# Performance work log

Hardware: AMD Instinct MI355X
Metric: run time of the kernel (lower is better)

## Reference

```python
import jax, jax.numpy as jnp
import numpy as np

C_RED = 8
BN_EPS = 1e-5
NORM_EPS = 1e-6

# pairwise upper-triangular index lists (static, matches torch buffers)
_idx_i, _idx_j = [], []
for _i in range(C_RED):
    for _j in range(_i, C_RED):
        _idx_i.append(_i)
        _idx_j.append(_j)
IDX_I = np.array(_idx_i, dtype=np.int32)
IDX_J = np.array(_idx_j, dtype=np.int32)


def setup_inputs() -> dict:
    key = jax.random.key(0)
    ks = jax.random.split(key, 8)
    B, Cin, H, W = 32, 256, 56, 56
    x = jax.random.normal(ks[0], (B, Cin, H, W), dtype=jnp.float32)
    w_reduce = jax.random.normal(ks[1], (C_RED, Cin, 1, 1), dtype=jnp.float32) * 0.05
    bn_gamma = jax.random.uniform(ks[2], (C_RED,), dtype=jnp.float32, minval=0.5, maxval=1.5)
    bn_beta = jax.random.normal(ks[3], (C_RED,), dtype=jnp.float32) * 0.1
    bn_mean = jax.random.normal(ks[4], (C_RED,), dtype=jnp.float32) * 0.1
    bn_var = jax.random.uniform(ks[5], (C_RED,), dtype=jnp.float32, minval=0.5, maxval=1.5)
    w_dw = jax.random.normal(ks[6], (C_RED, 1, 3, 3), dtype=jnp.float32) * 0.3
    scale = jax.random.uniform(ks[7], (1, C_RED, 1, 1), dtype=jnp.float32, minval=0.5, maxval=1.5)
    return {"x": x, "w_reduce": w_reduce, "bn_gamma": bn_gamma, "bn_beta": bn_beta,
            "bn_mean": bn_mean, "bn_var": bn_var, "w_dw": w_dw, "scale": scale}


def _l2norm_ch(z):
    # F.normalize(p=2, dim=1, eps=1e-6): x / max(||x||_2, eps)
    n = jnp.sqrt(jnp.sum(z * z, axis=1, keepdims=True))
    return z / jnp.maximum(n, NORM_EPS)


def reference(x, w_reduce, bn_gamma, bn_beta, bn_mean, bn_var, w_dw, scale):
    # 1x1 conv (no bias)
    z = jax.lax.conv_general_dilated(x, w_reduce, (1, 1), 'VALID',
                                     dimension_numbers=('NCHW', 'OIHW', 'NCHW'))
    # BatchNorm (inference) + ReLU
    inv = bn_gamma / jnp.sqrt(bn_var + BN_EPS)
    z = z * inv[None, :, None, None] + (bn_beta - bn_mean * inv)[None, :, None, None]
    z = jax.nn.relu(z)
    # depthwise 3x3 twist conv, padding 1, times per-channel scale
    z_twist = jax.lax.conv_general_dilated(z, w_dw, (1, 1), ((1, 1), (1, 1)),
                                           dimension_numbers=('NCHW', 'OIHW', 'NCHW'),
                                           feature_group_count=C_RED) * scale
    z_norm = _l2norm_ch(z)
    z_twist_norm = _l2norm_ch(z_twist)
    # gathered pairwise products over upper-triangular channel pairs
    interactions = jnp.take(z_norm, IDX_I, axis=1) * jnp.take(z_twist_norm, IDX_J, axis=1)
    return jnp.concatenate([z_norm, interactions], axis=1)  # [B, 8+36, H, W]
```

## Files before the change

### kernel.cpp

```cpp
#include <hip/hip_runtime.h>

#define BATCH 32
#define CIN   256
#define CR    8
#define HDIM  56
#define WDIM  56
#define HW    3136
#define COUT  44

#define TILE  256

__device__ __constant__ const int PI36[36] =
    {0,0,0,0,0,0,0,0, 1,1,1,1,1,1,1, 2,2,2,2,2,2, 3,3,3,3,3, 4,4,4,4, 5,5,5, 6,6, 7};
__device__ __constant__ const int PJ36[36] =
    {0,1,2,3,4,5,6,7, 1,2,3,4,5,6,7, 2,3,4,5,6,7, 3,4,5,6,7, 4,5,6,7, 5,6,7, 6,7, 7};

__global__ __launch_bounds__(512, 4) void k1_reduce_bn_relu(
    const float* __restrict__ x, const float* __restrict__ wr,
    const float* __restrict__ gamma, const float* __restrict__ beta,
    const float* __restrict__ mean, const float* __restrict__ var,
    float* __restrict__ z)
{
    const int tid  = threadIdx.x;
    const int lane = tid & 63;
    const int wv   = __builtin_amdgcn_readfirstlane(tid >> 6);
    const int px0  = blockIdx.x * TILE;
    const int gp   = px0 + 4 * lane;
    const int b    = gp / HW;
    const int p    = gp - b * HW;
    const int cin0 = wv * 32;

    const float* __restrict__ xq =
        x + (size_t)b * CIN * HW + (size_t)cin0 * HW + p;

    float acc[4][CR];
#pragma unroll
    for (int q = 0; q < 4; ++q)
#pragma unroll
        for (int c = 0; c < CR; ++c) acc[q][c] = 0.f;

    float4 xa[4], xb[4];
    auto loadx = [&](float4 (&arr)[4], int base) {
#pragma unroll
        for (int j = 0; j < 4; ++j)
            arr[j] = *reinterpret_cast<const float4*>(
                         xq + (size_t)(base + j) * HW);
    };
    auto consume = [&](const float4 (&arr)[4], int base) {
#pragma unroll
        for (int j = 0; j < 4; ++j) {
            const int cin = cin0 + base + j;
            const float px4[4] = {arr[j].x, arr[j].y, arr[j].z, arr[j].w};
#pragma unroll
            for (int c = 0; c < CR; ++c) {
                const float wgt = wr[c * CIN + cin];
#pragma unroll
                for (int q = 0; q < 4; ++q)
                    acc[q][c] = fmaf(px4[q], wgt, acc[q][c]);
            }
        }
    };

    loadx(xa, 0);
    loadx(xb, 4);
#pragma unroll
    for (int k0 = 0; k0 < 32; k0 += 8) {
        consume(xa, k0);
        if (k0 + 8  < 32) loadx(xa, k0 + 8);
        consume(xb, k0 + 4);
        if (k0 + 12 < 32) loadx(xb, k0 + 12);
    }

    __shared__ float pacc[8][CR][TILE];
#pragma unroll
    for (int c = 0; c < CR; ++c)
        *reinterpret_cast<float4*>(&pacc[wv][c][4 * lane]) =
            make_float4(acc[0][c], acc[1][c], acc[2][c], acc[3][c]);
    __syncthreads();

    const int c   = tid >> 6;
    const int pxb = tid & 63;
    const float inv = gamma[c] / sqrtf(var[c] + 1e-5f);
    const float sh  = beta[c] - mean[c] * inv;
#pragma unroll
    for (int k = 0; k < 4; ++k) {
        const int px = pxb + 64 * k;
        float s = 0.f;
#pragma unroll
        for (int w = 0; w < 8; ++w) s += pacc[w][c][px];
        z[(size_t)(px0 + px) * CR + c] = fmaxf(fmaf(s, inv, sh), 0.f);
    }
}

__global__ __launch_bounds__(256) void k2_dw_norm_inter(
    const float* __restrict__ z, const float* __restrict__ wdw,
    const float* __restrict__ scale, float* __restrict__ out)
{
    const int lane = threadIdx.x & 63;
    const int wv   = __builtin_amdgcn_readfirstlane(threadIdx.x >> 6);
    const int t = blockIdx.x * 64 + lane;
    const int b = t / HW;
    const int p = t - b * HW;
    const int h = p / WDIM;
    const int w = p - h * WDIM;

    const float* __restrict__ zimg = z + (size_t)b * HW * CR;

    float4 n0[9], n1[9];
    float  mk[9];
#pragma unroll
    for (int dy = -1; dy <= 1; ++dy) {
#pragma unroll
        for (int dx = -1; dx <= 1; ++dx) {
            const int k  = (dy + 1) * 3 + (dx + 1);
            const int hh = h + dy, ww = w + dx;
            const bool ok = (hh >= 0) & (hh < HDIM) & (ww >= 0) & (ww < WDIM);
            const int hc = min(max(hh, 0), HDIM - 1);
            const int wc = min(max(ww, 0), WDIM - 1);
            mk[k] = ok ? 1.0f : 0.0f;
            const float* zn = zimg + (size_t)(hc * WDIM + wc) * CR;
            n0[k] = reinterpret_cast<const float4*>(zn)[0];
            n1[k] = reinterpret_cast<const float4*>(zn)[1];
        }
    }

    const float zc[CR] = {n0[4].x, n0[4].y, n0[4].z, n0[4].w,
                          n1[4].x, n1[4].y, n1[4].z, n1[4].w};

    float tw[CR];
#pragma unroll
    for (int c = 0; c < CR; ++c) tw[c] = 0.f;
#pragma unroll
    for (int k = 0; k < 9; ++k) {
        const float nv[CR] = {n0[k].x, n0[k].y, n0[k].z, n0[k].w,
                              n1[k].x, n1[k].y, n1[k].z, n1[k].w};
#pragma unroll
        for (int c = 0; c < CR; ++c)
            tw[c] = fmaf(nv[c] * mk[k], wdw[c * 9 + k], tw[c]);
    }

    float s1 = 0.f, s2 = 0.f;
#pragma unroll
    for (int c = 0; c < CR; ++c) {
        tw[c] *= scale[c];
        s1 = fmaf(zc[c], zc[c], s1);
        s2 = fmaf(tw[c], tw[c], s2);
    }
    const float r1 = 1.0f / fmaxf(sqrtf(s1), 1e-6f);
    const float r2 = 1.0f / fmaxf(sqrtf(s2), 1e-6f);

    float a[CR], tb[CR];
#pragma unroll
    for (int c = 0; c < CR; ++c) { a[c] = zc[c] * r1; tb[c] = tw[c] * r2; }

    float* op = out + (size_t)b * COUT * HW + p;
#pragma unroll
    for (int c = 0; c < COUT; ++c) {
        if ((c / 11) == wv) {
            const float val = (c < CR) ? a[c]
                                       : a[PI36[c - CR]] * tb[PJ36[c - CR]];
            op[(size_t)c * HW] = val;
        }
    }
}

extern "C" void kernel_launch(void* const* d_in, const int* in_sizes, int n_in,
                              void* d_out, int out_size, void* d_ws, size_t ws_size,
                              hipStream_t stream) {
    const float* x     = (const float*)d_in[0];
    const float* wr    = (const float*)d_in[1];
    const float* gamma = (const float*)d_in[2];
    const float* beta  = (const float*)d_in[3];
    const float* mean  = (const float*)d_in[4];
    const float* var   = (const float*)d_in[5];
    const float* wdw   = (const float*)d_in[6];
    const float* scale = (const float*)d_in[7];
    float* out = (float*)d_out;
    float* z   = (float*)d_ws;

    const int npix = BATCH * HW;
    k1_reduce_bn_relu<<<npix / TILE, 512, 0, stream>>>(x, wr, gamma, beta, mean, var, z);
    k2_dw_norm_inter<<<npix / 64, 256, 0, stream>>>(z, wdw, scale, out);
}
```

Before: 175.3 us.

## Split reduce conv into per-channel-group partial kernel plus global reduction kernel

Replaces the single reduce+BN kernel with three kernels. A prep kernel transposes the 1x1 weights and precomputes the BN scale and shift. A partial kernel gives each block one batch and one 32-channel group over the whole image, with weights read as float4. A third kernel sums the 8 partials from global memory and applies BN and ReLU. This removes the shared-memory cross-wave reduction and per-block weight gathers, but adds about 25 MB of partial writes and reads to global memory plus two extra launches.

```diff
diff --git a/kernel.cpp b/kernel.cpp
--- a/kernel.cpp
+++ b/kernel.cpp
@@ -8,30 +8,47 @@
 #define HW    3136
 #define COUT  44
 
-#define TILE  256
+#define NCG   8
+#define CPG   32
+#define NPIX  (BATCH*HW)
+#define ZFLT  (NPIX*CR)
+#define F4PP  784
 
 __device__ __constant__ const int PI36[36] =
     {0,0,0,0,0,0,0,0, 1,1,1,1,1,1,1, 2,2,2,2,2,2, 3,3,3,3,3, 4,4,4,4, 5,5,5, 6,6, 7};
 __device__ __constant__ const int PJ36[36] =
     {0,1,2,3,4,5,6,7, 1,2,3,4,5,6,7, 2,3,4,5,6,7, 3,4,5,6,7, 4,5,6,7, 5,6,7, 6,7, 7};
 
-__global__ __launch_bounds__(512, 4) void k1_reduce_bn_relu(
-    const float* __restrict__ x, const float* __restrict__ wr,
-    const float* __restrict__ gamma, const float* __restrict__ beta,
-    const float* __restrict__ mean, const float* __restrict__ var,
-    float* __restrict__ z)
-{
-    const int tid  = threadIdx.x;
-    const int lane = tid & 63;
-    const int wv   = __builtin_amdgcn_readfirstlane(tid >> 6);
-    const int px0  = blockIdx.x * TILE;
-    const int gp   = px0 + 4 * lane;
-    const int b    = gp / HW;
-    const int p    = gp - b * HW;
-    const int cin0 = wv * 32;
-
-    const float* __restrict__ xq =
-        x + (size_t)b * CIN * HW + (size_t)cin0 * HW + p;
+__global__ __launch_bounds__(256) void k0_prep(
+    const float* __restrict__ wr, const float* __restrict__ gamma,
+    const float* __restrict__ beta, const float* __restrict__ mean,
+    const float* __restrict__ var,
+    float* __restrict__ wrT, float* __restrict__ invc, float* __restrict__ shc)
+{
+    const int t = threadIdx.x;
+#pragma unroll
+    for (int c = 0; c < CR; ++c) wrT[t * CR + c] = wr[c * CIN + t];
+    if (t < CR) {
+        const float iv = gamma[t] / sqrtf(var[t] + 1e-5f);
+        invc[t] = iv;
+        shc[t]  = beta[t] - mean[t] * iv;
+    }
+}
+
+__global__ __launch_bounds__(832) void k1a_partial(
+    const float* __restrict__ x, const float* __restrict__ wrT,
+    float* __restrict__ part)
+{
+    const int blk = blockIdx.x;
+    const int b   = blk >> 3;
+    const int cg  = blk & 7;
+    const int t   = threadIdx.x;
+    const bool act = (t < F4PP);
+
+    const float4* __restrict__ xs4 = reinterpret_cast<const float4*>(
+        x + ((size_t)b * CIN + (size_t)cg * CPG) * HW);
+    const float4* __restrict__ wt4 = reinterpret_cast<const float4*>(
+        wrT + (size_t)cg * CPG * CR);
 
     float acc[4][CR];
 #pragma unroll
@@ -39,57 +56,66 @@
 #pragma unroll
         for (int c = 0; c < CR; ++c) acc[q][c] = 0.f;
 
-    float4 xa[4], xb[4];
-    auto loadx = [&](float4 (&arr)[4], int base) {
-#pragma unroll
-        for (int j = 0; j < 4; ++j)
-            arr[j] = *reinterpret_cast<const float4*>(
-                         xq + (size_t)(base + j) * HW);
-    };
-    auto consume = [&](const float4 (&arr)[4], int base) {
-#pragma unroll
-        for (int j = 0; j < 4; ++j) {
-            const int cin = cin0 + base + j;
-            const float px4[4] = {arr[j].x, arr[j].y, arr[j].z, arr[j].w};
-#pragma unroll
-            for (int c = 0; c < CR; ++c) {
-                const float wgt = wr[c * CIN + cin];
-#pragma unroll
-                for (int q = 0; q < 4; ++q)
-                    acc[q][c] = fmaf(px4[q], wgt, acc[q][c]);
-            }
-        }
-    };
-
-    loadx(xa, 0);
-    loadx(xb, 4);
-#pragma unroll
-    for (int k0 = 0; k0 < 32; k0 += 8) {
-        consume(xa, k0);
-        if (k0 + 8  < 32) loadx(xa, k0 + 8);
-        consume(xb, k0 + 4);
-        if (k0 + 12 < 32) loadx(xb, k0 + 12);
-    }
-
-    __shared__ float pacc[8][CR][TILE];
-#pragma unroll
-    for (int c = 0; c < CR; ++c)
-        *reinterpret_cast<float4*>(&pacc[wv][c][4 * lane]) =
-            make_float4(acc[0][c], acc[1][c], acc[2][c], acc[3][c]);
-    __syncthreads();
-
-    const int c   = tid >> 6;
-    const int pxb = tid & 63;
-    const float inv = gamma[c] / sqrtf(var[c] + 1e-5f);
-    const float sh  = beta[c] - mean[c] * inv;
-#pragma unroll
-    for (int k = 0; k < 4; ++k) {
-        const int px = pxb + 64 * k;
-        float s = 0.f;
-#pragma unroll
-        for (int w = 0; w < 8; ++w) s += pacc[w][c][px];
-        z[(size_t)(px0 + px) * CR + c] = fmaxf(fmaf(s, inv, sh), 0.f);
-    }
+    float4 buf[4];
+    if (act) {
+#pragma unroll
+        for (int i = 0; i < 4; ++i) buf[i] = xs4[i * F4PP + t];
+    }
+
+    for (int k0 = 0; k0 < CPG; k0 += 4) {
+#pragma unroll
+        for (int i = 0; i < 4; ++i) {
+            const int cin = k0 + i;
+            const float4 w0 = wt4[2 * cin];
+            const float4 w1 = wt4[2 * cin + 1];
+            const float4 v  = buf[i];
+            const float px[4] = {v.x, v.y, v.z, v.w};
+            const float wc[CR] = {w0.x, w0.y, w0.z, w0.w,
+                                  w1.x, w1.y, w1.z, w1.w};
+#pragma unroll
+            for (int q = 0; q < 4; ++q)
+#pragma unroll
+                for (int c = 0; c < CR; ++c)
+                    acc[q][c] = fmaf(px[q], wc[c], acc[q][c]);
+            if (act && (k0 + 4 + i) < CPG)
+                buf[i] = xs4[(size_t)(k0 + 4 + i) * F4PP + t];
+        }
+    }
+
+    if (act) {
+        float* pp = part + (size_t)cg * ZFLT + ((size_t)b * HW + 4 * t) * CR;
+#pragma unroll
+        for (int q = 0; q < 4; ++q) {
+            *reinterpret_cast<float4*>(pp + q * CR) =
+                make_float4(acc[q][0], acc[q][1], acc[q][2], acc[q][3]);
+            *reinterpret_cast<float4*>(pp + q * CR + 4) =
+                make_float4(acc[q][4], acc[q][5], acc[q][6], acc[q][7]);
+        }
+    }
+}
+
+__global__ __launch_bounds__(512) void k1b_reduce_bn(
+    const float* __restrict__ part, const float* __restrict__ invc,
+    const float* __restrict__ shc, float* __restrict__ z)
+{
+    const int v = blockIdx.x * 512 + threadIdx.x;
+    const float4* __restrict__ p4 = reinterpret_cast<const float4*>(part);
+
+    float4 s = p4[v];
+#pragma unroll
+    for (int cg = 1; cg < NCG; ++cg) {
+        const float4 t4 = p4[(size_t)cg * (ZFLT / 4) + v];
+        s.x += t4.x; s.y += t4.y; s.z += t4.z; s.w += t4.w;
+    }
+    const int c0 = (v & 1) * 4;
+    const float4 iv = *reinterpret_cast<const float4*>(invc + c0);
+    const float4 sh = *reinterpret_cast<const float4*>(shc + c0);
+    float4 r;
+    r.x = fmaxf(fmaf(s.x, iv.x, sh.x), 0.f);
+    r.y = fmaxf(fmaf(s.y, iv.y, sh.y), 0.f);
+    r.z = fmaxf(fmaf(s.z, iv.z, sh.z), 0.f);
+    r.w = fmaxf(fmaf(s.w, iv.w, sh.w), 0.f);
+    reinterpret_cast<float4*>(z)[v] = r;
 }
 
 __global__ __launch_bounds__(256) void k2_dw_norm_inter(
@@ -176,9 +202,16 @@
     const float* wdw   = (const float*)d_in[6];
     const float* scale = (const float*)d_in[7];
     float* out = (float*)d_out;
-    float* z   = (float*)d_ws;
-
-    const int npix = BATCH * HW;
-    k1_reduce_bn_relu<<<npix / TILE, 512, 0, stream>>>(x, wr, gamma, beta, mean, var, z);
-    k2_dw_norm_inter<<<npix / 64, 256, 0, stream>>>(z, wdw, scale, out);
-}
+
+    float* ws   = (float*)d_ws;
+    float* z    = ws;
+    float* part = ws + ZFLT;
+    float* wrT  = ws + (size_t)ZFLT * 9;
+    float* invc = wrT + 2048;
+    float* shc  = invc + 8;
+
+    k0_prep<<<1, 256, 0, stream>>>(wr, gamma, beta, mean, var, wrT, invc, shc);
+    k1a_partial<<<BATCH * NCG, 832, 0, stream>>>(x, wrT, part);
+    k1b_reduce_bn<<<ZFLT / 4 / 512, 512, 0, stream>>>(part, invc, shc, z);
+    k2_dw_norm_inter<<<NPIX / 64, 256, 0, stream>>>(z, wdw, scale, out);
+}
```

Result: slower. 208.4 us (+18.9%).
